# Performance work log

Measured on AMD Instinct MI355X. Metric: run time of the kernel, lower is better.

Reference implementation:

```python
import jax, jax.numpy as jnp
import numpy as np
import math

# SH band constants (match torch source)
A0C0 = math.pi * (1.0 / math.sqrt(4.0 * math.pi))
A1C1 = (2.0 * math.pi / math.sqrt(3.0)) * (math.sqrt(3.0) / math.sqrt(4.0 * math.pi))
A2C2 = (2.0 * math.pi / math.sqrt(8.0)) * (3.0 * math.sqrt(5.0) / math.sqrt(12.0 * math.pi))
AMBIENT = 0.8
SIGMA = 1e-4   # BlendParams defaults
GAMMA = 1e-4
BG = (1.0, 1.0, 1.0)
ZNEAR, ZFAR = 1.0, 100.0
EPS = 1e-10

V, F = 100000, 200000
N, H, W, K = 2, 512, 512, 8


def setup_inputs() -> dict:
    key = jax.random.key(0)
    ks = jax.random.split(key, 8)
    verts_normals = jax.random.normal(ks[0], (V, 3), dtype=jnp.float32)
    verts_colors = jax.random.uniform(ks[1], (V, 3), dtype=jnp.float32)
    sh_coeffs = jax.random.normal(ks[2], (1, 9, 3), dtype=jnp.float32) * 0.3
    bary = jax.random.uniform(ks[3], (N, H, W, K, 3), dtype=jnp.float32) + 1e-3
    bary_coords = bary / jnp.sum(bary, axis=-1, keepdims=True)  # convex weights
    zbuf = ZNEAR + (ZFAR - ZNEAR) * jax.random.uniform(ks[4], (N, H, W, K), dtype=jnp.float32)
    dists = jax.random.normal(ks[5], (N, H, W, K), dtype=jnp.float32) * 1e-4  # signed pixel-to-edge dists
    faces = jax.random.randint(ks[6], (F, 3), 0, V, dtype=jnp.int64 if jax.config.jax_enable_x64 else jnp.int32)
    pix_to_face = jax.random.randint(ks[7], (N, H, W, K), -20000, F,
                                     dtype=jnp.int64 if jax.config.jax_enable_x64 else jnp.int32)
    return {"verts_normals": verts_normals, "verts_colors": verts_colors,
            "sh_coeffs": sh_coeffs, "bary_coords": bary_coords,
            "zbuf": zbuf, "dists": dists, "faces": faces, "pix_to_face": pix_to_face}


def _forward(verts_normals, verts_colors, sh_coeffs, bary_coords, zbuf, dists,
             faces, pix_to_face):
    # --- per-vertex SH shading ---
    sh = sh_coeffs.at[..., 0, :].add(AMBIENT)          # (1,9,3), ambient term
    nrm = jnp.maximum(jnp.linalg.norm(verts_normals, axis=-1, keepdims=True), 1e-6)
    n = verts_normals / nrm                            # (V,3)
    nx, ny, nz = n[..., 0], n[..., 1], n[..., 2]
    Y = jnp.stack([
        jnp.full(nx.shape, A0C0, dtype=n.dtype),
        -A1C1 * ny,
        A1C1 * nz,
        -A1C1 * nx,
        A2C2 * nx * ny,
        -A2C2 * ny * nz,
        A2C2 * 0.5 / math.sqrt(3.0) * (3.0 * nz * nz - 1.0),
        -A2C2 * nx * nz,
        A2C2 * 0.5 * (nx * nx - ny * ny),
    ], axis=-1)                                        # (V,9)
    shading = jnp.einsum('vn,nc->vc', Y, sh[0])        # (V,3)
    verts_colors_shaded = verts_colors * shading       # (V,3)

    # --- face gather + barycentric interpolation ---
    face_colors = verts_colors_shaded[faces]           # (F,3,3)
    mask = pix_to_face >= 0                            # (N,H,W,K)
    idx = jnp.where(mask, pix_to_face, 0)
    pix_face_vals = face_colors[idx]                   # (N,H,W,K,3,3)
    colors = jnp.sum(bary_coords[..., None] * pix_face_vals, axis=-2)  # (N,H,W,K,3)
    colors = jnp.where(mask[..., None], colors, 0.0)

    # --- softmax RGB blend ---
    maskf = mask.astype(colors.dtype)
    prob = jax.nn.sigmoid(-dists / SIGMA) * maskf                       # (N,H,W,K)
    alpha = jnp.prod(1.0 - prob, axis=-1)                               # (N,H,W)
    z_inv = (ZFAR - zbuf) / (ZFAR - ZNEAR) * maskf
    z_inv_max = jnp.maximum(jnp.max(z_inv, axis=-1, keepdims=True), EPS)
    weights_num = prob * jnp.exp((z_inv - z_inv_max) / GAMMA)
    delta = jnp.exp((EPS - z_inv_max) / GAMMA)                          # background weight
    denom = jnp.sum(weights_num, axis=-1, keepdims=True) + delta
    weighted_colors = jnp.sum(weights_num[..., None] * colors, axis=-2)  # (N,H,W,3)
    bg = jnp.asarray(BG, dtype=colors.dtype)
    rgb = (weighted_colors + delta * bg) / denom
    return jnp.concatenate([rgb, (1.0 - alpha)[..., None]], axis=-1)    # (N,H,W,4)


def reference(verts_normals, verts_colors, sh_coeffs, bary_coords, zbuf, dists,
              faces, pix_to_face):
    return _forward(verts_normals, verts_colors, sh_coeffs, bary_coords, zbuf,
                    dists, faces, pix_to_face)
```

## Files before the change

kernel.cpp:

```cpp
#include <hip/hip_runtime.h>
#include <math.h>

namespace {

constexpr float kA0C0    = 0.8862269254527580f;
constexpr float kA1C1    = 1.7724538509055159f;
constexpr float kA2C2    = 2.4270324670f;
constexpr float kAmbient = 0.8f;
constexpr float kInvSigma = 1e4f;
constexpr float kInvGamma = 1e4f;
constexpr float kEps     = 1e-10f;
constexpr float kZnear   = 1.0f;
constexpr float kZfar    = 100.0f;
constexpr int   kK       = 8;

__global__ void shade_verts_kernel(const float* __restrict__ vn,
                                   const float* __restrict__ vc,
                                   const float* __restrict__ sh,
                                   float* __restrict__ vs, int V) {
  int v = blockIdx.x * blockDim.x + threadIdx.x;
  if (v >= V) return;
  float nx = vn[3 * v + 0], ny = vn[3 * v + 1], nz = vn[3 * v + 2];
  float nrm = fmaxf(sqrtf(nx * nx + ny * ny + nz * nz), 1e-6f);
  nx /= nrm; ny /= nrm; nz /= nrm;
  float Y[9];
  Y[0] = kA0C0;
  Y[1] = -kA1C1 * ny;
  Y[2] =  kA1C1 * nz;
  Y[3] = -kA1C1 * nx;
  Y[4] =  kA2C2 * nx * ny;
  Y[5] = -kA2C2 * ny * nz;
  Y[6] =  kA2C2 * (0.5f / 1.7320508075688772f) * (3.0f * nz * nz - 1.0f);
  Y[7] = -kA2C2 * nx * nz;
  Y[8] =  kA2C2 * 0.5f * (nx * nx - ny * ny);
#pragma unroll
  for (int c = 0; c < 3; ++c) {
    float s = Y[0] * (sh[0 * 3 + c] + kAmbient);
#pragma unroll
    for (int n = 1; n < 9; ++n) s += Y[n] * sh[n * 3 + c];
    vs[3 * v + c] = vc[3 * v + c] * s;
  }
}

__global__ void face_colors_kernel(const int* __restrict__ faces,
                                   const float* __restrict__ vs,
                                   float4* __restrict__ fc4, int F) {
  int f = blockIdx.x * blockDim.x + threadIdx.x;
  if (f >= F) return;
  int i0 = faces[3 * f + 0], i1 = faces[3 * f + 1], i2 = faces[3 * f + 2];
  fc4[3 * f + 0] = make_float4(vs[3 * i0], vs[3 * i0 + 1], vs[3 * i0 + 2], 0.f);
  fc4[3 * f + 1] = make_float4(vs[3 * i1], vs[3 * i1 + 1], vs[3 * i1 + 2], 0.f);
  fc4[3 * f + 2] = make_float4(vs[3 * i2], vs[3 * i2 + 1], vs[3 * i2 + 2], 0.f);
}

__global__ void __launch_bounds__(256) blend_kernel(
    const float* __restrict__ bary,
    const float* __restrict__ zbuf,
    const float* __restrict__ dists,
    const int* __restrict__ p2f,
    const float4* __restrict__ fc4,
    float4* __restrict__ out, int total) {
  int t = blockIdx.x * blockDim.x + threadIdx.x;
  if (t >= total) return;
  int k = t & 7;

  int   f = p2f[t];
  float z = zbuf[t];
  float d = dists[t];
  float b0 = bary[3 * t + 0];
  float b1 = bary[3 * t + 1];
  float b2 = bary[3 * t + 2];

  bool m = f >= 0;
  float pr = m ? __frcp_rn(1.0f + expf(d * kInvSigma)) : 0.0f;
  float zi = m ? (kZfar - z) * (1.0f / (kZfar - kZnear)) : 0.0f;

  float maxz = zi;
#pragma unroll
  for (int s = 1; s < 8; s <<= 1) maxz = fmaxf(maxz, __shfl_xor(maxz, s));
  maxz = fmaxf(maxz, kEps);

  float one_m = 1.0f - pr;
#pragma unroll
  for (int s = 1; s < 8; s <<= 1) one_m *= __shfl_xor(one_m, s);

  float w = pr * expf((zi - maxz) * kInvGamma);
  float delta = expf((kEps - maxz) * kInvGamma);

  float cr = 0.0f, cg = 0.0f, cb = 0.0f;
  if (w != 0.0f) {
    const float4* fp = fc4 + 3 * f;
    float4 v0 = fp[0], v1 = fp[1], v2 = fp[2];
    cr = w * (b0 * v0.x + b1 * v1.x + b2 * v2.x);
    cg = w * (b0 * v0.y + b1 * v1.y + b2 * v2.y);
    cb = w * (b0 * v0.z + b1 * v1.z + b2 * v2.z);
  }

  float denom = w;
#pragma unroll
  for (int s = 1; s < 8; s <<= 1) {
    denom += __shfl_xor(denom, s);
    cr    += __shfl_xor(cr, s);
    cg    += __shfl_xor(cg, s);
    cb    += __shfl_xor(cb, s);
  }

  if (k == 0) {
    denom += delta;
    float inv = __frcp_rn(denom);
    float4 o;
    o.x = (cr + delta) * inv;
    o.y = (cg + delta) * inv;
    o.z = (cb + delta) * inv;
    o.w = 1.0f - one_m;
    out[t >> 3] = o;
  }
}

}

extern "C" void kernel_launch(void* const* d_in, const int* in_sizes, int n_in,
                              void* d_out, int out_size, void* d_ws, size_t ws_size,
                              hipStream_t stream) {
  const float* vn    = (const float*)d_in[0];
  const float* vc    = (const float*)d_in[1];
  const float* sh    = (const float*)d_in[2];
  const float* bary  = (const float*)d_in[3];
  const float* zbuf  = (const float*)d_in[4];
  const float* dists = (const float*)d_in[5];
  const int*   faces = (const int*)d_in[6];
  const int*   p2f   = (const int*)d_in[7];
  float*       out   = (float*)d_out;

  const int V = in_sizes[0] / 3;
  const int F = in_sizes[6] / 3;
  const int total = in_sizes[4];

  float* vs = (float*)d_ws;
  size_t vsBytes = (size_t)V * 3 * sizeof(float);
  size_t fcOff   = (vsBytes + 255) & ~(size_t)255;
  float4* fc4    = (float4*)((char*)d_ws + fcOff);

  shade_verts_kernel<<<(V + 255) / 256, 256, 0, stream>>>(vn, vc, sh, vs, V);
  face_colors_kernel<<<(F + 255) / 256, 256, 0, stream>>>(faces, vs, fc4, F);
  blend_kernel<<<(total + 255) / 256, 256, 0, stream>>>(
      bary, zbuf, dists, p2f, fc4, (float4*)out, total);
}
```

Baseline: 154.7 us.

## Fuse vertex shading into face kernel, store fp16 face colors, thread-per-pixel blend

Merges vertex shading and face-color gathering into one kernel that recomputes SH shading per face corner and writes the face colors as half-precision vectors. The blend kernel now gives each pixel to one thread, which loads its 8 samples with vector nontemporal loads and reduces them in registers instead of with cross-lane shuffles. It also switches to fast exp and writes the output with a nontemporal store. The aim is to drop a kernel launch and its intermediate buffer, halve the gather traffic for face colors, and cut shuffle overhead, at the cost of repeated shading work, fp16 rounding of colors, and strided bary loads per thread.

```diff
diff --git a/kernel.cpp b/kernel.cpp
--- a/kernel.cpp
+++ b/kernel.cpp
@@ -1,120 +1,115 @@
 #include <hip/hip_runtime.h>
 #include <math.h>
 
+typedef float    f4  __attribute__((ext_vector_type(4)));
+typedef int      i4  __attribute__((ext_vector_type(4)));
+typedef _Float16 hf4 __attribute__((ext_vector_type(4)));
+
 namespace {
 
-constexpr float kA0C0    = 0.8862269254527580f;
-constexpr float kA1C1    = 1.7724538509055159f;
-constexpr float kA2C2    = 2.4270324670f;
-constexpr float kAmbient = 0.8f;
+constexpr float kA0C0     = 0.8862269254527580f;
+constexpr float kA1C1     = 1.7724538509055159f;
+constexpr float kA2C2     = 2.4270324670f;
+constexpr float kAmbient  = 0.8f;
 constexpr float kInvSigma = 1e4f;
 constexpr float kInvGamma = 1e4f;
-constexpr float kEps     = 1e-10f;
-constexpr float kZnear   = 1.0f;
-constexpr float kZfar    = 100.0f;
-constexpr int   kK       = 8;
+constexpr float kEps      = 1e-10f;
+constexpr float kZfar     = 100.0f;
+constexpr float kInvZrng  = 1.0f / 99.0f;
 
-__global__ void shade_verts_kernel(const float* __restrict__ vn,
-                                   const float* __restrict__ vc,
-                                   const float* __restrict__ sh,
-                                   float* __restrict__ vs, int V) {
-  int v = blockIdx.x * blockDim.x + threadIdx.x;
-  if (v >= V) return;
-  float nx = vn[3 * v + 0], ny = vn[3 * v + 1], nz = vn[3 * v + 2];
-  float nrm = fmaxf(sqrtf(nx * nx + ny * ny + nz * nz), 1e-6f);
-  nx /= nrm; ny /= nrm; nz /= nrm;
-  float Y[9];
-  Y[0] = kA0C0;
-  Y[1] = -kA1C1 * ny;
-  Y[2] =  kA1C1 * nz;
-  Y[3] = -kA1C1 * nx;
-  Y[4] =  kA2C2 * nx * ny;
-  Y[5] = -kA2C2 * ny * nz;
-  Y[6] =  kA2C2 * (0.5f / 1.7320508075688772f) * (3.0f * nz * nz - 1.0f);
-  Y[7] = -kA2C2 * nx * nz;
-  Y[8] =  kA2C2 * 0.5f * (nx * nx - ny * ny);
-#pragma unroll
-  for (int c = 0; c < 3; ++c) {
-    float s = Y[0] * (sh[0 * 3 + c] + kAmbient);
-#pragma unroll
-    for (int n = 1; n < 9; ++n) s += Y[n] * sh[n * 3 + c];
-    vs[3 * v + c] = vc[3 * v + c] * s;
-  }
-}
-
-__global__ void face_colors_kernel(const int* __restrict__ faces,
-                                   const float* __restrict__ vs,
-                                   float4* __restrict__ fc4, int F) {
+__global__ void shade_face_kernel(const float* __restrict__ vn,
+                                  const float* __restrict__ vc,
+                                  const float* __restrict__ sh,
+                                  const int* __restrict__ faces,
+                                  hf4* __restrict__ fc, int F) {
   int f = blockIdx.x * blockDim.x + threadIdx.x;
   if (f >= F) return;
-  int i0 = faces[3 * f + 0], i1 = faces[3 * f + 1], i2 = faces[3 * f + 2];
-  fc4[3 * f + 0] = make_float4(vs[3 * i0], vs[3 * i0 + 1], vs[3 * i0 + 2], 0.f);
-  fc4[3 * f + 1] = make_float4(vs[3 * i1], vs[3 * i1 + 1], vs[3 * i1 + 2], 0.f);
-  fc4[3 * f + 2] = make_float4(vs[3 * i2], vs[3 * i2 + 1], vs[3 * i2 + 2], 0.f);
+  float s0r = sh[0] + kAmbient, s0g = sh[1] + kAmbient, s0b = sh[2] + kAmbient;
+  int vid[3] = {faces[3 * f + 0], faces[3 * f + 1], faces[3 * f + 2]};
+#pragma unroll
+  for (int j = 0; j < 3; ++j) {
+    int v = vid[j];
+    float nx = vn[3 * v + 0], ny = vn[3 * v + 1], nz = vn[3 * v + 2];
+    float nrm = fmaxf(sqrtf(nx * nx + ny * ny + nz * nz), 1e-6f);
+    nx /= nrm; ny /= nrm; nz /= nrm;
+    float Y1 = -kA1C1 * ny, Y2 = kA1C1 * nz, Y3 = -kA1C1 * nx;
+    float Y4 =  kA2C2 * nx * ny, Y5 = -kA2C2 * ny * nz;
+    float Y6 =  kA2C2 * (0.5f / 1.7320508075688772f) * (3.0f * nz * nz - 1.0f);
+    float Y7 = -kA2C2 * nx * nz, Y8 = kA2C2 * 0.5f * (nx * nx - ny * ny);
+    float r = kA0C0 * s0r + Y1 * sh[3] + Y2 * sh[6]  + Y3 * sh[9]  + Y4 * sh[12]
+            + Y5 * sh[15] + Y6 * sh[18] + Y7 * sh[21] + Y8 * sh[24];
+    float g = kA0C0 * s0g + Y1 * sh[4] + Y2 * sh[7]  + Y3 * sh[10] + Y4 * sh[13]
+            + Y5 * sh[16] + Y6 * sh[19] + Y7 * sh[22] + Y8 * sh[25];
+    float b = kA0C0 * s0b + Y1 * sh[5] + Y2 * sh[8]  + Y3 * sh[11] + Y4 * sh[14]
+            + Y5 * sh[17] + Y6 * sh[20] + Y7 * sh[23] + Y8 * sh[26];
+    hf4 o;
+    o.x = (_Float16)(vc[3 * v + 0] * r);
+    o.y = (_Float16)(vc[3 * v + 1] * g);
+    o.z = (_Float16)(vc[3 * v + 2] * b);
+    o.w = (_Float16)0.0f;
+    fc[3 * f + j] = o;
+  }
 }
 
 __global__ void __launch_bounds__(256) blend_kernel(
     const float* __restrict__ bary,
-    const float* __restrict__ zbuf,
-    const float* __restrict__ dists,
-    const int* __restrict__ p2f,
-    const float4* __restrict__ fc4,
-    float4* __restrict__ out, int total) {
-  int t = blockIdx.x * blockDim.x + threadIdx.x;
-  if (t >= total) return;
-  int k = t & 7;
+    const f4* __restrict__ zb4,
+    const f4* __restrict__ ds4,
+    const i4* __restrict__ pf4,
+    const hf4* __restrict__ fc,
+    f4* __restrict__ out, int P) {
+  int p = blockIdx.x * blockDim.x + threadIdx.x;
+  if (p >= P) return;
 
-  int   f = p2f[t];
-  float z = zbuf[t];
-  float d = dists[t];
-  float b0 = bary[3 * t + 0];
-  float b1 = bary[3 * t + 1];
-  float b2 = bary[3 * t + 2];
+  i4 fA = __builtin_nontemporal_load(pf4 + 2 * p);
+  i4 fB = __builtin_nontemporal_load(pf4 + 2 * p + 1);
+  f4 zA = __builtin_nontemporal_load(zb4 + 2 * p);
+  f4 zB = __builtin_nontemporal_load(zb4 + 2 * p + 1);
+  f4 dA = __builtin_nontemporal_load(ds4 + 2 * p);
+  f4 dB = __builtin_nontemporal_load(ds4 + 2 * p + 1);
+  int   fk[8] = {fA.x, fA.y, fA.z, fA.w, fB.x, fB.y, fB.z, fB.w};
+  float z[8]  = {zA.x, zA.y, zA.z, zA.w, zB.x, zB.y, zB.z, zB.w};
+  float d[8]  = {dA.x, dA.y, dA.z, dA.w, dB.x, dB.y, dB.z, dB.w};
 
-  bool m = f >= 0;
-  float pr = m ? __frcp_rn(1.0f + expf(d * kInvSigma)) : 0.0f;
-  float zi = m ? (kZfar - z) * (1.0f / (kZfar - kZnear)) : 0.0f;
-
-  float maxz = zi;
+  float pr[8], zi[8];
+  float maxz = kEps, alpha = 1.0f;
 #pragma unroll
-  for (int s = 1; s < 8; s <<= 1) maxz = fmaxf(maxz, __shfl_xor(maxz, s));
-  maxz = fmaxf(maxz, kEps);
-
-  float one_m = 1.0f - pr;
-#pragma unroll
-  for (int s = 1; s < 8; s <<= 1) one_m *= __shfl_xor(one_m, s);
-
-  float w = pr * expf((zi - maxz) * kInvGamma);
-  float delta = expf((kEps - maxz) * kInvGamma);
-
-  float cr = 0.0f, cg = 0.0f, cb = 0.0f;
-  if (w != 0.0f) {
-    const float4* fp = fc4 + 3 * f;
-    float4 v0 = fp[0], v1 = fp[1], v2 = fp[2];
-    cr = w * (b0 * v0.x + b1 * v1.x + b2 * v2.x);
-    cg = w * (b0 * v0.y + b1 * v1.y + b2 * v2.y);
-    cb = w * (b0 * v0.z + b1 * v1.z + b2 * v2.z);
+  for (int k = 0; k < 8; ++k) {
+    bool m = fk[k] >= 0;
+    float e = __expf(d[k] * kInvSigma);
+    float prv = m ? 1.0f / (1.0f + e) : 0.0f;
+    pr[k] = prv;
+    alpha *= 1.0f - prv;
+    float zv = m ? (kZfar - z[k]) * kInvZrng : 0.0f;
+    zi[k] = zv;
+    maxz = fmaxf(maxz, zv);
   }
 
-  float denom = w;
+  float delta = __expf((kEps - maxz) * kInvGamma);
+  float denom = delta;
+  float cr = 0.0f, cg = 0.0f, cb = 0.0f;
 #pragma unroll
-  for (int s = 1; s < 8; s <<= 1) {
-    denom += __shfl_xor(denom, s);
-    cr    += __shfl_xor(cr, s);
-    cg    += __shfl_xor(cg, s);
-    cb    += __shfl_xor(cb, s);
+  for (int k = 0; k < 8; ++k) {
+    float w = pr[k] * __expf((zi[k] - maxz) * kInvGamma);
+    denom += w;
+    if (w != 0.0f) {
+      int t = 8 * p + k;
+      float b0 = bary[3 * t + 0], b1 = bary[3 * t + 1], b2 = bary[3 * t + 2];
+      hf4 v0 = fc[3 * fk[k] + 0];
+      hf4 v1 = fc[3 * fk[k] + 1];
+      hf4 v2 = fc[3 * fk[k] + 2];
+      cr += w * (b0 * (float)v0.x + b1 * (float)v1.x + b2 * (float)v2.x);
+      cg += w * (b0 * (float)v0.y + b1 * (float)v1.y + b2 * (float)v2.y);
+      cb += w * (b0 * (float)v0.z + b1 * (float)v1.z + b2 * (float)v2.z);
+    }
   }
 
-  if (k == 0) {
-    denom += delta;
-    float inv = __frcp_rn(denom);
-    float4 o;
-    o.x = (cr + delta) * inv;
-    o.y = (cg + delta) * inv;
-    o.z = (cb + delta) * inv;
-    o.w = 1.0f - one_m;
-    out[t >> 3] = o;
-  }
+  f4 o;
+  o.x = (cr + delta) / denom;
+  o.y = (cg + delta) / denom;
+  o.z = (cb + delta) / denom;
+  o.w = 1.0f - alpha;
+  __builtin_nontemporal_store(o, out + p);
 }
 
 }
@@ -130,19 +125,13 @@
   const float* dists = (const float*)d_in[5];
   const int*   faces = (const int*)d_in[6];
   const int*   p2f   = (const int*)d_in[7];
-  float*       out   = (float*)d_out;
 
-  const int V = in_sizes[0] / 3;
   const int F = in_sizes[6] / 3;
-  const int total = in_sizes[4];
+  const int P = in_sizes[4] / 8;
 
-  float* vs = (float*)d_ws;
-  size_t vsBytes = (size_t)V * 3 * sizeof(float);
-  size_t fcOff   = (vsBytes + 255) & ~(size_t)255;
-  float4* fc4    = (float4*)((char*)d_ws + fcOff);
+  hf4* fc = (hf4*)d_ws;
 
-  shade_verts_kernel<<<(V + 255) / 256, 256, 0, stream>>>(vn, vc, sh, vs, V);
-  face_colors_kernel<<<(F + 255) / 256, 256, 0, stream>>>(faces, vs, fc4, F);
-  blend_kernel<<<(total + 255) / 256, 256, 0, stream>>>(
-      bary, zbuf, dists, p2f, fc4, (float4*)out, total);
+  shade_face_kernel<<<(F + 255) / 256, 256, 0, stream>>>(vn, vc, sh, faces, fc, F);
+  blend_kernel<<<(P + 255) / 256, 256, 0, stream>>>(
+      bary, (const f4*)zbuf, (const f4*)dists, (const i4*)p2f, fc, (f4*)d_out, P);
 }
```

Result: faster. 149.9 us (-3.1%).
